# Performance work log

Hardware: AMD Instinct MI355X
Metric: run time of the kernel (lower is better)

The kernel has to match this reference:

```python
import jax, jax.numpy as jnp
import numpy as np

B, L, D_MODEL = 2, 4096, 1024
D_STATE, D_CONV, EXPAND, HEADDIM = 128, 4, 2, 64
D_INNER = EXPAND * D_MODEL              # 2048
NHEADS = D_INNER // HEADDIM             # 32
CONV_DIM = D_INNER + 2 * D_STATE        # 2304 (ngroups=1)
D_IN_PROJ = 2 * D_INNER + 2 * D_STATE + NHEADS  # 4384
CHUNK = 128
EPS = 1e-5


def _segsum(a):
    # a: (..., T) log-decays -> (..., T, T) lower-triangular segment sums, -inf above diagonal
    T = a.shape[-1]
    cs = jnp.cumsum(a, axis=-1)
    seg = cs[..., :, None] - cs[..., None, :]
    mask = jnp.tril(jnp.ones((T, T), dtype=bool))
    return jnp.where(mask, seg, -jnp.inf)


def _forward(x, norm_w, norm_b, in_proj_w, conv_w, conv_b, dt_bias, A_log, D, rms_w, out_proj_w):
    b, l, _ = x.shape
    # pre-LayerNorm
    mu = jnp.mean(x, -1, keepdims=True)
    var = jnp.mean(jnp.square(x - mu), -1, keepdims=True)
    xn = (x - mu) * jax.lax.rsqrt(var + EPS) * norm_w + norm_b
    zxbcdt = xn @ in_proj_w.T                              # (b,l,D_IN_PROJ)
    z = zxbcdt[..., :D_INNER]
    xBC = zxbcdt[..., D_INNER:D_INNER + CONV_DIM]
    dt = jax.nn.softplus(zxbcdt[..., -NHEADS:] + dt_bias)  # (b,l,h)
    # causal depthwise conv1d + SiLU over (x, B, C)
    xc = jnp.pad(xBC.transpose(0, 2, 1), ((0, 0), (0, 0), (D_CONV - 1, 0)))
    xc = jax.lax.conv_general_dilated(xc, conv_w[:, None, :], (1,), 'VALID',
                                      feature_group_count=CONV_DIM,
                                      dimension_numbers=('NCH', 'OIH', 'NCH'))
    xBC = jax.nn.silu(xc + conv_b[None, :, None]).transpose(0, 2, 1)
    xs = xBC[..., :D_INNER].reshape(b, l, NHEADS, HEADDIM)
    Bm = xBC[..., D_INNER:D_INNER + D_STATE]               # (b,l,n)
    Cm = xBC[..., D_INNER + D_STATE:]                      # (b,l,n)
    # SSD chunked selective scan
    A = -jnp.exp(A_log)                                    # (h,)
    a = dt * A                                             # (b,l,h) log decay
    X = xs * dt[..., None]                                 # (b,l,h,p)
    c = l // CHUNK
    a_c = a.reshape(b, c, CHUNK, NHEADS).transpose(0, 3, 1, 2)   # (b,h,c,s)
    a_cum = jnp.cumsum(a_c, -1)
    Lmat = jnp.exp(_segsum(a_c))                           # (b,h,c,s,s)
    Xc = X.reshape(b, c, CHUNK, NHEADS, HEADDIM)
    Bc = Bm.reshape(b, c, CHUNK, D_STATE)
    Cc = Cm.reshape(b, c, CHUNK, D_STATE)
    # intra-chunk (diagonal block) output
    Y_diag = jnp.einsum('bcln,bcsn,bhcls,bcshp->bclhp', Cc, Bc, Lmat, Xc)
    # chunk-final states
    decay_states = jnp.exp(a_cum[..., -1:] - a_cum)        # (b,h,c,s)
    states = jnp.einsum('bcln,bhcl,bclhp->bchpn', Bc, decay_states, Xc)
    states = jnp.concatenate([jnp.zeros_like(states[:, :1]), states], axis=1)
    chunk_decay = jnp.exp(_segsum(jnp.pad(a_cum[..., -1], ((0, 0), (0, 0), (1, 0)))))  # (b,h,c+1,c+1)
    prev = jnp.einsum('bhzc,bchpn->bzhpn', chunk_decay, states)[:, :-1]  # (b,c,h,p,n)
    # inter-chunk (off-diagonal) output
    Y_off = jnp.einsum('bcln,bchpn,bhcl->bclhp', Cc, prev, jnp.exp(a_cum))
    y = (Y_diag + Y_off).reshape(b, l, NHEADS, HEADDIM) + D[None, None, :, None] * xs
    y = y.reshape(b, l, D_INNER)
    # gated RMSNorm (norm_before_gate=False): norm(y * silu(z))
    y = y * jax.nn.silu(z)
    y = y * jax.lax.rsqrt(jnp.mean(jnp.square(y), -1, keepdims=True) + EPS) * rms_w
    return x + y @ out_proj_w.T


def setup_inputs() -> dict:
    key = jax.random.key(0)
    ks = jax.random.split(key, 8)
    return {
        'x': jax.random.normal(ks[0], (B, L, D_MODEL), jnp.float32),
        'norm_w': jnp.ones((D_MODEL,), jnp.float32),
        'norm_b': jnp.zeros((D_MODEL,), jnp.float32),
        'in_proj_w': 0.02 * jax.random.normal(ks[1], (D_IN_PROJ, D_MODEL), jnp.float32),
        'conv_w': 0.2 * jax.random.normal(ks[2], (CONV_DIM, D_CONV), jnp.float32),
        'conv_b': jnp.zeros((CONV_DIM,), jnp.float32),
        'dt_bias': jax.random.uniform(ks[3], (NHEADS,), jnp.float32, -4.0, 0.0),
        'A_log': jnp.log(jax.random.uniform(ks[4], (NHEADS,), jnp.float32, 1.0, 16.0)),
        'D': jnp.ones((NHEADS,), jnp.float32),
        'rms_w': jnp.ones((D_INNER,), jnp.float32),
        'out_proj_w': 0.02 * jax.random.normal(ks[5], (D_MODEL, D_INNER), jnp.float32),
    }


def reference(x, norm_w, norm_b, in_proj_w, conv_w, conv_b, dt_bias, A_log, D, rms_w, out_proj_w):
    return _forward(x, norm_w, norm_b, in_proj_w, conv_w, conv_b, dt_bias, A_log, D, rms_w, out_proj_w)
```

## Files before the change

### kernel.cpp

```cpp
#include <hip/hip_runtime.h>

#define B_ 2
#define L_ 4096
#define DMODEL 1024
#define DSTATE 128
#define DINNER 2048
#define NH 32
#define HD 64
#define DPROJ 4384
#define DPROJP 4480
#define NC 32
#define EPSF 1e-5f
#define ROWS (B_*L_)

typedef unsigned short u16;
typedef __attribute__((ext_vector_type(8))) short s8v;
typedef __attribute__((ext_vector_type(4))) float f4v;
typedef __attribute__((ext_vector_type(4))) int i4v;
typedef __attribute__((ext_vector_type(2))) int i2v;
typedef __attribute__((ext_vector_type(4))) float fl4;

static __device__ __forceinline__ float b2f(u16 u){
  unsigned int x = ((unsigned int)u) << 16;
  return __builtin_bit_cast(float, x);
}
static __device__ __forceinline__ u16 f2b(float f){
  unsigned int x = __builtin_bit_cast(unsigned int, f);
  unsigned int r = x + 0x7FFFu + ((x >> 16) & 1u);
  return (u16)(r >> 16);
}
static __device__ __forceinline__ float softplusf(float x){
  return (x > 20.f) ? x : log1pf(expf(x));
}
static __device__ __forceinline__ void gl_lds16(const u16* g, u16* l){
  __builtin_amdgcn_global_load_lds(
    (const __attribute__((address_space(1))) unsigned int*)g,
    (__attribute__((address_space(3))) unsigned int*)l, 16, 0, 0);
}
static __device__ __forceinline__ int swz(int row, int col){
  return row*128 + ((((col >> 3) ^ (row & 15)) << 3) | (col & 7));
}
static __device__ __forceinline__ int swz64(int row, int col){
  return row*64 + ((((col >> 3) ^ (row & 7)) << 3) | (col & 7));
}
static __device__ __forceinline__ int osw(int t, int j){
  return t*64 + ((((j >> 3) ^ ((t >> 3) & 7)) << 3) | (j & 7));
}

__global__ void k_dbg(float* out, float v){ out[0] = v; }

__global__ __launch_bounds__(256) void k_pack_w1(const float* __restrict__ W, u16* __restrict__ Wb){
  size_t i = (size_t)blockIdx.x*256 + threadIdx.x;
  if (i >= (size_t)DPROJP*DMODEL) return;
  size_t n = i / DMODEL;
  Wb[i] = (n < DPROJ) ? f2b(W[i]) : (u16)0;
}
__global__ __launch_bounds__(256) void k_pack_w2(const float* __restrict__ W, u16* __restrict__ Wb){
  size_t i = (size_t)blockIdx.x*256 + threadIdx.x;
  if (i >= (size_t)DMODEL*DINNER) return;
  Wb[i] = f2b(W[i]);
}

__global__ __launch_bounds__(256) void k_ln(const float* __restrict__ x, const float* __restrict__ nw,
                                            const float* __restrict__ nb, u16* __restrict__ xn){
  int m = blockIdx.x; int tid = threadIdx.x;
  const float* row = x + (size_t)m*DMODEL;
  fl4 v = *(const fl4*)&row[tid*4];
  float s1 = v[0]+v[1]+v[2]+v[3];
  float s2 = v[0]*v[0]+v[1]*v[1]+v[2]*v[2]+v[3]*v[3];
  #pragma unroll
  for (int o=32;o;o>>=1){ s1 += __shfl_down(s1,o); s2 += __shfl_down(s2,o); }
  __shared__ float r1[4], r2[4];
  if ((tid&63)==0){ r1[tid>>6]=s1; r2[tid>>6]=s2; }
  __syncthreads();
  s1 = r1[0]+r1[1]+r1[2]+r1[3]; s2 = r2[0]+r2[1]+r2[2]+r2[3];
  float mu = s1 * (1.f/DMODEL);
  float var = s2 * (1.f/DMODEL) - mu*mu;
  float rs = rsqrtf(var + EPSF);
  u16* o = xn + (size_t)m*DMODEL + tid*4;
  #pragma unroll
  for (int k=0;k<4;k++)
    o[k] = f2b((v[k]-mu)*rs*nw[tid*4+k] + nb[tid*4+k]);
}

template<int MODE>
__global__ __launch_bounds__(256) void k_gemm(const u16* __restrict__ A, const u16* __restrict__ Bw,
                  void* __restrict__ Cout, const float* __restrict__ resid,
                  int K, int lda, int ldb, int ldc){
  __shared__ u16 smem[2*128*64];
  u16* sA = smem;
  u16* sB = smem + 128*64;
  int tid = threadIdx.x;
  int ln = tid & 63, wid = tid >> 6;
  int wr = wid >> 1, wc = wid & 1;
  size_t m0 = (size_t)blockIdx.x * 128, n0 = (size_t)blockIdx.y * 128;
  int lrow = ln >> 3;
  f4v acc[4][4] = {};
  for (int k0 = 0; k0 < K; k0 += 64){
    #pragma unroll
    for (int i = 0; i < 4; ++i){
      int seg = wid*4 + i;
      int row = seg*8 + lrow;
      int scol = ((ln & 7) ^ (row & 7)) * 8;
      gl_lds16(&A [(m0+row)*lda + k0 + scol], &sA[seg*512]);
      gl_lds16(&Bw[(n0+row)*ldb + k0 + scol], &sB[seg*512]);
    }
    __syncthreads();
    #pragma unroll
    for (int kk=0; kk<2; kk++){
      s8v af[4], bfr[4];
      #pragma unroll
      for (int t=0;t<4;t++){
        int col = kk*32 + (ln>>4)*8;
        af[t]  = *(const s8v*)&sA[swz64(wr*64+t*16+(ln&15), col)];
        bfr[t] = *(const s8v*)&sB[swz64(wc*64+t*16+(ln&15), col)];
      }
      #pragma unroll
      for (int mt=0;mt<4;mt++)
        #pragma unroll
        for (int nt=0;nt<4;nt++)
          acc[mt][nt] = __builtin_amdgcn_mfma_f32_16x16x32_bf16(af[mt], bfr[nt], acc[mt][nt], 0,0,0);
    }
    __syncthreads();
  }
  if (MODE == 0){
    #pragma unroll
    for (int mt=0;mt<4;mt++)
      #pragma unroll
      for (int nt=0;nt<4;nt++)
        #pragma unroll
        for (int j=0;j<4;j++){
          int m = wr*64 + mt*16 + (ln>>4)*4 + j;
          int n = wc*64 + nt*16 + (ln&15);
          smem[m*128 + n] = f2b(acc[mt][nt][j]);
        }
    __syncthreads();
    #pragma unroll
    for (int it = 0; it < 8; ++it){
      int idx = (tid + it*256)*8;
      int row = idx >> 7, col = idx & 127;
      *(i4v*)&((u16*)Cout)[(m0+row)*ldc + n0 + col] = *(const i4v*)&smem[idx];
    }
  } else {
    #pragma unroll
    for (int mt=0;mt<4;mt++)
      #pragma unroll
      for (int nt=0;nt<4;nt++)
        #pragma unroll
        for (int j=0;j<4;j++){
          size_t m = m0 + wr*64 + mt*16 + (ln>>4)*4 + j;
          size_t n = n0 + wc*64 + nt*16 + (ln&15);
          ((float*)Cout)[m*ldc + n] = acc[mt][nt][j] + resid[m*ldc + n];
        }
  }
}

__global__ __launch_bounds__(256) void k_conv(const u16* __restrict__ zx, const float* __restrict__ cw,
    const float* __restrict__ cb, const float* __restrict__ dtb,
    u16* __restrict__ Xt, u16* __restrict__ Bln, u16* __restrict__ Bt,
    u16* __restrict__ Cln, float* __restrict__ dtg){
  __shared__ u16 in_s[131*64];
  __shared__ u16 out_s[128*64];
  __shared__ float dt_s[128];
  int bid = blockIdx.x;
  int g = bid % 36;
  int c = (bid / 36) & 31;
  int b = bid / (36*32);
  int tid = threadIdx.x;
  int t0 = c*128;
  size_t rowb = (size_t)b*L_ + t0;
  for (int i8 = tid; i8 < 1048; i8 += 256){
    int r = i8 >> 3, j0 = (i8 & 7)*8;
    int t = t0 - 3 + r;
    i4v v;
    if (t >= 0) v = *(const i4v*)&zx[((size_t)b*L_ + t)*DPROJP + 2048 + g*64 + j0];
    else { v[0]=0; v[1]=0; v[2]=0; v[3]=0; }
    *(i4v*)&in_s[r*64 + j0] = v;
  }
  if (g < 32 && tid < 128){
    float raw = b2f(zx[(rowb + tid)*DPROJP + (DPROJ - NH) + g]);
    float d = softplusf(raw + dtb[g]);
    dt_s[tid] = d;
    dtg[(size_t)(b*NH + g)*L_ + t0 + tid] = d;
  }
  __syncthreads();
  {
    int j = tid & 63;
    int ch = g*64 + j;
    float w0 = cw[ch*4+0], w1 = cw[ch*4+1], w2 = cw[ch*4+2], w3 = cw[ch*4+3];
    float bia = cb[ch];
    int tb = tid >> 6;
    #pragma unroll
    for (int it = 0; it < 32; ++it){
      int t = tb + it*4;
      float a = bia
        + w0*b2f(in_s[(t+0)*64 + j]) + w1*b2f(in_s[(t+1)*64 + j])
        + w2*b2f(in_s[(t+2)*64 + j]) + w3*b2f(in_s[(t+3)*64 + j]);
      out_s[osw(t, j)] = f2b(a / (1.f + __expf(-a)));
    }
  }
  __syncthreads();
  if (g < 32){
    for (int i = tid; i < 1024; i += 256){
      int j = i >> 4, tb = (i & 15)*8;
      i4v o; u16* ou = (u16*)&o;
      #pragma unroll
      for (int k = 0; k < 8; ++k)
        ou[k] = f2b(b2f(out_s[osw(tb + k, j)]) * dt_s[tb + k]);
      *(i4v*)&Xt[((size_t)((b*NH + g)*HD + j))*L_ + t0 + tb] = o;
    }
  } else {
    int q = g - 32;
    for (int i = tid; i < 1024; i += 256){
      int t = i >> 3, j0 = (i & 7)*8;
      i4v v = *(const i4v*)&out_s[osw(t, j0)];
      if (q < 2) *(i4v*)&Bln[(rowb + t)*DSTATE + q*64 + j0] = v;
      else       *(i4v*)&Cln[(rowb + t)*DSTATE + (q-2)*64 + j0] = v;
    }
    if (q < 2){
      for (int i = tid; i < 1024; i += 256){
        int j = i >> 4, tb = (i & 15)*8;
        i4v o; u16* ou = (u16*)&o;
        #pragma unroll
        for (int k = 0; k < 8; ++k) ou[k] = out_s[osw(tb + k, j)];
        *(i4v*)&Bt[((size_t)(b*DSTATE + q*64 + j))*L_ + t0 + tb] = o;
      }
    }
  }
}

__global__ __launch_bounds__(128) void k_acum(const float* __restrict__ dtg, const float* __restrict__ A_log,
                                              float* __restrict__ acum){
  int bid = blockIdx.x;
  int c = bid & 31, h = (bid >> 5) & 31, b = bid >> 10;
  int l = threadIdx.x;
  __shared__ float a[128];
  float Ah = -expf(A_log[h]);
  a[l] = dtg[(size_t)(b*NH + h)*L_ + c*128 + l] * Ah;
  __syncthreads();
  #pragma unroll
  for (int d = 1; d < 128; d <<= 1){
    float v = (l >= d) ? a[l-d] : 0.f;
    __syncthreads();
    a[l] += v;
    __syncthreads();
  }
  acum[(size_t)bid*128 + l] = a[l];
}

__global__ __launch_bounds__(256) void k_states(const u16* __restrict__ Xt, const u16* __restrict__ Bt,
    const float* __restrict__ acum, u16* __restrict__ states){
  __shared__ u16 sX[64*128];
  __shared__ u16 sB[128*128];
  __shared__ float dec[128];
  int bid = blockIdx.x;
  int h = bid & 31, c = (bid >> 5) & 31, b = bid >> 10;
  int tid = threadIdx.x;
  const float* acg = acum + ((size_t)((b*NH + h)*NC + c))*128;
  if (tid < 128) dec[tid] = __expf(acg[127] - acg[tid]);
  __syncthreads();
  const u16* xtb = Xt + ((size_t)((b*NH + h)*HD))*L_ + c*128;
  for (int i = tid*8; i < 64*128; i += 256*8){
    int p = i >> 7, l0 = i & 127;
    i4v v = *(const i4v*)&xtb[(size_t)p*L_ + l0];
    const u16* vu = (const u16*)&v;
    i4v o; u16* ou = (u16*)&o;
    #pragma unroll
    for (int j = 0; j < 8; ++j) ou[j] = f2b(b2f(vu[j]) * dec[l0 + j]);
    *(i4v*)&sX[swz(p, l0)] = o;
  }
  const u16* btb = Bt + (size_t)(b*DSTATE)*L_ + c*128;
  for (int i = tid*8; i < 128*128; i += 256*8){
    int n = i >> 7, l0 = i & 127;
    *(i4v*)&sB[swz(n, l0)] = *(const i4v*)&btb[(size_t)n*L_ + l0];
  }
  __syncthreads();
  int ln = tid & 63, wid = tid >> 6;
  int wr = wid >> 1, wc = wid & 1;
  f4v acc[2][4] = {};
  #pragma unroll
  for (int kk = 0; kk < 4; ++kk){
    s8v af[2], bfr[4];
    int col = kk*32 + (ln>>4)*8;
    #pragma unroll
    for (int t = 0; t < 2; ++t)
      af[t] = *(const s8v*)&sX[swz(wr*32 + t*16 + (ln&15), col)];
    #pragma unroll
    for (int t = 0; t < 4; ++t)
      bfr[t] = *(const s8v*)&sB[swz(wc*64 + t*16 + (ln&15), col)];
    #pragma unroll
    for (int mt = 0; mt < 2; ++mt)
      #pragma unroll
      for (int nt = 0; nt < 4; ++nt)
        acc[mt][nt] = __builtin_amdgcn_mfma_f32_16x16x32_bf16(af[mt], bfr[nt], acc[mt][nt], 0,0,0);
  }
  u16* out = states + ((size_t)((b*NC + c)*NH + h))*(HD*DSTATE);
  #pragma unroll
  for (int mt = 0; mt < 2; ++mt)
    #pragma unroll
    for (int nt = 0; nt < 4; ++nt){
      int n = wc*64 + nt*16 + (ln&15);
      #pragma unroll
      for (int j = 0; j < 4; ++j){
        int p = wr*32 + mt*16 + (ln>>4)*4 + j;
        out[(size_t)p*DSTATE + n] = f2b(acc[mt][nt][j]);
      }
    }
}

__global__ __launch_bounds__(256) void k_scan(u16* __restrict__ states, const float* __restrict__ acum){
  int bid = blockIdx.x;
  int eb = bid & 7;
  int hb = bid >> 3;
  int h = hb & 31, b = hb >> 5;
  int tid = threadIdx.x;
  size_t ebase = (size_t)eb*1024 + (size_t)tid*4;
  size_t hoff = ((size_t)(b*NC*NH + h))*(HD*DSTATE) + ebase;
  float dec[NC];
  #pragma unroll
  for (int c = 0; c < NC; ++c)
    dec[c] = __expf(acum[((size_t)((b*NH + h)*NC + c))*128 + 127]);
  i2v w[NC];
  #pragma unroll
  for (int c = 0; c < NC; ++c)
    w[c] = *(const i2v*)&states[(size_t)c*(NH*HD*DSTATE) + hoff];
  float run[4] = {0.f, 0.f, 0.f, 0.f};
  #pragma unroll
  for (int c = 0; c < NC; ++c){
    u16* wu = (u16*)&w[c];
    #pragma unroll
    for (int j = 0; j < 4; ++j){
      float tmp = b2f(wu[j]);
      wu[j] = f2b(run[j]);
      run[j] = run[j]*dec[c] + tmp;
    }
  }
  #pragma unroll
  for (int c = 0; c < NC; ++c)
    *(i2v*)&states[(size_t)c*(NH*HD*DSTATE) + hoff] = w[c];
}

__global__ __launch_bounds__(256) void k_y(const u16* __restrict__ Cln, const u16* __restrict__ Bln,
    const u16* __restrict__ Xt, const u16* __restrict__ prev, const float* __restrict__ acum,
    const float* __restrict__ dtg, const float* __restrict__ Dp, u16* __restrict__ Y){
  __shared__ u16 sC[128*128];
  __shared__ u16 sBS[128*128];
  __shared__ float dt_s[128];
  int bid = blockIdx.x;
  int h = bid & 31, c = (bid >> 5) & 31, b = bid >> 10;
  int tid = threadIdx.x;
  size_t rowb = (size_t)b*L_ + c*128;
  const float* acg = acum + ((size_t)((b*NH + h)*NC + c))*128;
  if (tid < 128) dt_s[tid] = dtg[(size_t)(b*NH + h)*L_ + c*128 + tid];
  for (int i = tid*8; i < 128*128; i += 256*8){
    int row = i >> 7, col = i & 127;
    int d = swz(row, col);
    *(i4v*)&sC[d]  = *(const i4v*)&Cln[(rowb + row)*DSTATE + col];
    *(i4v*)&sBS[d] = *(const i4v*)&Bln[(rowb + row)*DSTATE + col];
  }
  __syncthreads();
  int ln = tid & 63, wid = tid >> 6;
  int wr = wid >> 1, wc = wid & 1;
  float Dh = Dp[h];
  f4v aS[4][4] = {};
  #pragma unroll
  for (int kk = 0; kk < 4; ++kk){
    s8v af[4], bfr[4];
    #pragma unroll
    for (int t = 0; t < 4; ++t){
      int col = kk*32 + (ln>>4)*8;
      af[t]  = *(const s8v*)&sC [swz(wr*64 + t*16 + (ln&15), col)];
      bfr[t] = *(const s8v*)&sBS[swz(wc*64 + t*16 + (ln&15), col)];
    }
    #pragma unroll
    for (int mt = 0; mt < 4; ++mt)
      #pragma unroll
      for (int nt = 0; nt < 4; ++nt)
        aS[mt][nt] = __builtin_amdgcn_mfma_f32_16x16x32_bf16(af[mt], bfr[nt], aS[mt][nt], 0,0,0);
  }
  __syncthreads();
  #pragma unroll
  for (int mt = 0; mt < 4; ++mt)
    #pragma unroll
    for (int nt = 0; nt < 4; ++nt){
      int s = wc*64 + nt*16 + (ln&15);
      float as = acg[s];
      #pragma unroll
      for (int j = 0; j < 4; ++j){
        int l = wr*64 + mt*16 + (ln>>4)*4 + j;
        float v = 0.f;
        if (s <= l){
          v = aS[mt][nt][j] * __expf(acg[l] - as);
          if (s == l) v += Dh / dt_s[l];
        }
        sBS[swz(l, s)] = f2b(v);
      }
    }
  __syncthreads();
  const u16* xtb = Xt + ((size_t)((b*NH + h)*HD))*L_ + c*128;
  const u16* pv = prev + ((size_t)((b*NC + c)*NH + h))*(HD*DSTATE);
  f4v aD[4][2] = {}, aO[4][2] = {};
  #pragma unroll
  for (int kk = 0; kk < 4; ++kk){
    s8v aSf[4], aCf[4], bXf[2], bPf[2];
    #pragma unroll
    for (int t = 0; t < 4; ++t){
      int col = kk*32 + (ln>>4)*8;
      int row = wr*64 + t*16 + (ln&15);
      aSf[t] = *(const s8v*)&sBS[swz(row, col)];
      aCf[t] = *(const s8v*)&sC[swz(row, col)];
    }
    #pragma unroll
    for (int t = 0; t < 2; ++t){
      int p = wc*32 + t*16 + (ln&15);
      int ko = kk*32 + (ln>>4)*8;
      bXf[t] = *(const s8v*)&xtb[(size_t)p*L_ + ko];
      bPf[t] = *(const s8v*)&pv[(size_t)p*DSTATE + ko];
    }
    #pragma unroll
    for (int mt = 0; mt < 4; ++mt)
      #pragma unroll
      for (int nt = 0; nt < 2; ++nt){
        aD[mt][nt] = __builtin_amdgcn_mfma_f32_16x16x32_bf16(aSf[mt], bXf[nt], aD[mt][nt], 0,0,0);
        aO[mt][nt] = __builtin_amdgcn_mfma_f32_16x16x32_bf16(aCf[mt], bPf[nt], aO[mt][nt], 0,0,0);
      }
  }
  __syncthreads();
  #pragma unroll
  for (int mt = 0; mt < 4; ++mt)
    #pragma unroll
    for (int nt = 0; nt < 2; ++nt){
      int p = wc*32 + nt*16 + (ln&15);
      #pragma unroll
      for (int j = 0; j < 4; ++j){
        int l = wr*64 + mt*16 + (ln>>4)*4 + j;
        float ex = __expf(acg[l]);
        float yv = aD[mt][nt][j] + ex*aO[mt][nt][j];
        sC[l*64 + (p ^ ((l & 7) << 3))] = f2b(yv);
      }
    }
  __syncthreads();
  #pragma unroll
  for (int it = 0; it < 4; ++it){
    int idx = (tid + it*256)*8;
    int row = idx >> 6, col0 = idx & 63;
    i4v v = *(const i4v*)&sC[row*64 + (col0 ^ ((row & 7) << 3))];
    *(i4v*)&Y[(rowb + row)*DINNER + h*HD + col0] = v;
  }
}

__global__ __launch_bounds__(256) void k_gate(u16* __restrict__ Y, const u16* __restrict__ zx,
                                              const float* __restrict__ rw){
  size_t m = blockIdx.x; int tid = threadIdx.x;
  u16* yrow = Y + m*DINNER + tid*8;
  const u16* zrow = zx + m*DPROJP + tid*8;
  i4v yv = *(const i4v*)yrow;
  i4v zv = *(const i4v*)zrow;
  const u16* yu = (const u16*)&yv;
  const u16* zu = (const u16*)&zv;
  float yg[8]; float ss = 0.f;
  #pragma unroll
  for (int k = 0; k < 8; ++k){
    float z = b2f(zu[k]);
    float g = z / (1.f + __expf(-z));
    float v = b2f(yu[k]) * g;
    yg[k] = v; ss += v*v;
  }
  #pragma unroll
  for (int o = 32; o; o >>= 1) ss += __shfl_down(ss, o);
  __shared__ float r[4];
  if ((tid&63) == 0) r[tid>>6] = ss;
  __syncthreads();
  ss = r[0]+r[1]+r[2]+r[3];
  float rstd = rsqrtf(ss*(1.f/DINNER) + EPSF);
  #pragma unroll
  for (int k = 0; k < 8; ++k)
    yrow[k] = f2b(yg[k]*rstd*rw[tid*8+k]);
}

extern "C" void kernel_launch(void* const* d_in, const int* in_sizes, int n_in,
                              void* d_out, int out_size, void* d_ws, size_t ws_size,
                              hipStream_t stream){
  const float* x        = (const float*)d_in[0];
  const float* norm_w   = (const float*)d_in[1];
  const float* norm_b   = (const float*)d_in[2];
  const float* in_proj  = (const float*)d_in[3];
  const float* conv_w   = (const float*)d_in[4];
  const float* conv_b   = (const float*)d_in[5];
  const float* dt_bias  = (const float*)d_in[6];
  const float* A_log    = (const float*)d_in[7];
  const float* Dp       = (const float*)d_in[8];
  const float* rms_w    = (const float*)d_in[9];
  const float* out_proj = (const float*)d_in[10];

  char* ws = (char*)d_ws;
  size_t off = 0;
  auto alloc = [&](size_t bytes) -> void* {
    void* p = ws + off;
    off += (bytes + 255) & ~(size_t)255;
    return p;
  };
  u16*   w1b    = (u16*)  alloc((size_t)DPROJP*DMODEL*2);
  u16*   w2b    = (u16*)  alloc((size_t)DMODEL*DINNER*2);
  u16*   xn     = (u16*)  alloc((size_t)ROWS*DMODEL*2);
  u16*   zx     = (u16*)  alloc((size_t)ROWS*DPROJP*2);
  u16*   Xt     = (u16*)  alloc((size_t)B_*NH*HD*L_*2);
  u16*   Bln    = (u16*)  alloc((size_t)ROWS*DSTATE*2);
  u16*   Bt     = (u16*)  alloc((size_t)B_*DSTATE*L_*2);
  u16*   Cln    = (u16*)  alloc((size_t)ROWS*DSTATE*2);
  float* dtg    = (float*)alloc((size_t)B_*NH*L_*4);
  float* acum   = (float*)alloc((size_t)B_*NH*NC*128*4);
  u16*   Y      = (u16*)  alloc((size_t)ROWS*DINNER*2);
  u16* states = (u16*)d_out;
  if (off > ws_size){
    k_dbg<<<1, 1, 0, stream>>>((float*)d_out, (float)ws_size);
    return;
  }

  k_pack_w1<<<dim3((DPROJP*DMODEL + 255)/256), 256, 0, stream>>>(in_proj, w1b);
  k_pack_w2<<<dim3((DMODEL*DINNER + 255)/256), 256, 0, stream>>>(out_proj, w2b);
  k_ln<<<dim3(ROWS), 256, 0, stream>>>(x, norm_w, norm_b, xn);
  k_gemm<0><<<dim3(ROWS/128, DPROJP/128), 256, 0, stream>>>(xn, w1b, zx, nullptr,
                                                            DMODEL, DMODEL, DMODEL, DPROJP);
  k_conv<<<dim3(B_*NC*36), 256, 0, stream>>>(zx, conv_w, conv_b, dt_bias,
                                             Xt, Bln, Bt, Cln, dtg);
  k_acum<<<dim3(B_*NH*NC), 128, 0, stream>>>(dtg, A_log, acum);
  k_states<<<dim3(B_*NC*NH), 256, 0, stream>>>(Xt, Bt, acum, states);
  k_scan<<<dim3(B_*NH*8), 256, 0, stream>>>(states, acum);
  k_y<<<dim3(B_*NC*NH), 256, 0, stream>>>(Cln, Bln, Xt, states, acum, dtg, Dp, Y);
  k_gate<<<dim3(ROWS), 256, 0, stream>>>(Y, zx, rms_w);
  k_gemm<1><<<dim3(ROWS/128, DMODEL/128), 256, 0, stream>>>(Y, w2b, d_out, x,
                                                            DINNER, DINNER, DINNER, DMODEL);
}
```

Before: 307.1 us.

## Fuse weight packing and chunk cumsum; remap GEMM tiles across XCDs

The two weight-packing kernels become one launch, and the per-chunk cumulative decay scan moves from its own kernel into the conv kernel, which already computes dt. Both GEMMs switch to a 1D grid whose block index is remapped so that consecutive tiles land on the same XCD (8-way interleave), aiming for better L2 reuse of A and B panels. The conv kernel now carries extra barriers for the scan, and its four extra B/C blocks per chunk run the scan on zeros.

```diff
diff --git a/kernel.cpp b/kernel.cpp
--- a/kernel.cpp
+++ b/kernel.cpp
@@ -49,16 +49,18 @@
 
 __global__ void k_dbg(float* out, float v){ out[0] = v; }
 
-__global__ __launch_bounds__(256) void k_pack_w1(const float* __restrict__ W, u16* __restrict__ Wb){
+#define NW1 ((size_t)DPROJP*DMODEL)
+#define NW2 ((size_t)DMODEL*DINNER)
+__global__ __launch_bounds__(256) void k_pack(const float* __restrict__ W1, const float* __restrict__ W2,
+                                              u16* __restrict__ W1b, u16* __restrict__ W2b){
   size_t i = (size_t)blockIdx.x*256 + threadIdx.x;
-  if (i >= (size_t)DPROJP*DMODEL) return;
-  size_t n = i / DMODEL;
-  Wb[i] = (n < DPROJ) ? f2b(W[i]) : (u16)0;
-}
-__global__ __launch_bounds__(256) void k_pack_w2(const float* __restrict__ W, u16* __restrict__ Wb){
-  size_t i = (size_t)blockIdx.x*256 + threadIdx.x;
-  if (i >= (size_t)DMODEL*DINNER) return;
-  Wb[i] = f2b(W[i]);
+  if (i < NW1){
+    size_t n = i / DMODEL;
+    W1b[i] = (n < DPROJ) ? f2b(W1[i]) : (u16)0;
+  } else if (i < NW1 + NW2){
+    size_t j = i - NW1;
+    W2b[j] = f2b(W2[j]);
+  }
 }
 
 __global__ __launch_bounds__(256) void k_ln(const float* __restrict__ x, const float* __restrict__ nw,
@@ -83,17 +85,17 @@
     o[k] = f2b((v[k]-mu)*rs*nw[tid*4+k] + nb[tid*4+k]);
 }
 
-template<int MODE>
-__global__ __launch_bounds__(256) void k_gemm(const u16* __restrict__ A, const u16* __restrict__ Bw,
-                  void* __restrict__ Cout, const float* __restrict__ resid,
-                  int K, int lda, int ldb, int ldc){
+__global__ __launch_bounds__(256) void k_gemm_in(const u16* __restrict__ A, const u16* __restrict__ Bw,
+                  u16* __restrict__ Cout, int K, int lda, int ldb, int ldc, int nwg, int mtiles){
   __shared__ u16 smem[2*128*64];
   u16* sA = smem;
   u16* sB = smem + 128*64;
+  int cpx = nwg >> 3;
+  int lin = (blockIdx.x & 7)*cpx + (blockIdx.x >> 3);
   int tid = threadIdx.x;
   int ln = tid & 63, wid = tid >> 6;
   int wr = wid >> 1, wc = wid & 1;
-  size_t m0 = (size_t)blockIdx.x * 128, n0 = (size_t)blockIdx.y * 128;
+  size_t m0 = (size_t)(lin % mtiles) * 128, n0 = (size_t)(lin / mtiles) * 128;
   int lrow = ln >> 3;
   f4v acc[4][4] = {};
   for (int k0 = 0; k0 < K; k0 += 64){
@@ -123,45 +125,85 @@
     }
     __syncthreads();
   }
-  if (MODE == 0){
-    #pragma unroll
-    for (int mt=0;mt<4;mt++)
-      #pragma unroll
-      for (int nt=0;nt<4;nt++)
+  #pragma unroll
+  for (int mt=0;mt<4;mt++)
+    #pragma unroll
+    for (int nt=0;nt<4;nt++)
+      #pragma unroll
+      for (int j=0;j<4;j++){
+        int m = wr*64 + mt*16 + (ln>>4)*4 + j;
+        int n = wc*64 + nt*16 + (ln&15);
+        smem[m*128 + n] = f2b(acc[mt][nt][j]);
+      }
+  __syncthreads();
+  #pragma unroll
+  for (int it = 0; it < 8; ++it){
+    int idx = (tid + it*256)*8;
+    int row = idx >> 7, col = idx & 127;
+    *(i4v*)&Cout[(m0+row)*ldc + n0 + col] = *(const i4v*)&smem[idx];
+  }
+}
+
+__global__ __launch_bounds__(256) void k_gemm_out(const u16* __restrict__ A, const u16* __restrict__ Bw,
+                  float* __restrict__ Cout, const float* __restrict__ resid,
+                  int K, int lda, int ldb, int ldc, int nwg, int mtiles){
+  __shared__ u16 sA[128*64];
+  __shared__ u16 sB[128*64];
+  int cpx = nwg >> 3;
+  int lin = (blockIdx.x & 7)*cpx + (blockIdx.x >> 3);
+  int tid = threadIdx.x;
+  int ln = tid & 63, wid = tid >> 6;
+  int wr = wid >> 1, wc = wid & 1;
+  size_t m0 = (size_t)(lin % mtiles) * 128, n0 = (size_t)(lin / mtiles) * 128;
+  int lrow = ln >> 3;
+  f4v acc[4][4] = {};
+  for (int k0 = 0; k0 < K; k0 += 64){
+    #pragma unroll
+    for (int i = 0; i < 4; ++i){
+      int seg = wid*4 + i;
+      int row = seg*8 + lrow;
+      int scol = ((ln & 7) ^ (row & 7)) * 8;
+      gl_lds16(&A [(m0+row)*lda + k0 + scol], &sA[seg*512]);
+      gl_lds16(&Bw[(n0+row)*ldb + k0 + scol], &sB[seg*512]);
+    }
+    __syncthreads();
+    #pragma unroll
+    for (int kk=0; kk<2; kk++){
+      s8v af[4], bfr[4];
+      #pragma unroll
+      for (int t=0;t<4;t++){
+        int col = kk*32 + (ln>>4)*8;
+        af[t]  = *(const s8v*)&sA[swz64(wr*64+t*16+(ln&15), col)];
+        bfr[t] = *(const s8v*)&sB[swz64(wc*64+t*16+(ln&15), col)];
+      }
+      #pragma unroll
+      for (int mt=0;mt<4;mt++)
         #pragma unroll
-        for (int j=0;j<4;j++){
-          int m = wr*64 + mt*16 + (ln>>4)*4 + j;
-          int n = wc*64 + nt*16 + (ln&15);
-          smem[m*128 + n] = f2b(acc[mt][nt][j]);
-        }
+        for (int nt=0;nt<4;nt++)
+          acc[mt][nt] = __builtin_amdgcn_mfma_f32_16x16x32_bf16(af[mt], bfr[nt], acc[mt][nt], 0,0,0);
+    }
     __syncthreads();
-    #pragma unroll
-    for (int it = 0; it < 8; ++it){
-      int idx = (tid + it*256)*8;
-      int row = idx >> 7, col = idx & 127;
-      *(i4v*)&((u16*)Cout)[(m0+row)*ldc + n0 + col] = *(const i4v*)&smem[idx];
-    }
-  } else {
-    #pragma unroll
-    for (int mt=0;mt<4;mt++)
-      #pragma unroll
-      for (int nt=0;nt<4;nt++)
-        #pragma unroll
-        for (int j=0;j<4;j++){
-          size_t m = m0 + wr*64 + mt*16 + (ln>>4)*4 + j;
-          size_t n = n0 + wc*64 + nt*16 + (ln&15);
-          ((float*)Cout)[m*ldc + n] = acc[mt][nt][j] + resid[m*ldc + n];
-        }
-  }
+  }
+  #pragma unroll
+  for (int mt=0;mt<4;mt++)
+    #pragma unroll
+    for (int nt=0;nt<4;nt++)
+      #pragma unroll
+      for (int j=0;j<4;j++){
+        size_t m = m0 + wr*64 + mt*16 + (ln>>4)*4 + j;
+        size_t n = n0 + wc*64 + nt*16 + (ln&15);
+        Cout[m*ldc + n] = acc[mt][nt][j] + resid[m*ldc + n];
+      }
 }
 
 __global__ __launch_bounds__(256) void k_conv(const u16* __restrict__ zx, const float* __restrict__ cw,
-    const float* __restrict__ cb, const float* __restrict__ dtb,
+    const float* __restrict__ cb, const float* __restrict__ dtb, const float* __restrict__ A_log,
     u16* __restrict__ Xt, u16* __restrict__ Bln, u16* __restrict__ Bt,
-    u16* __restrict__ Cln, float* __restrict__ dtg){
+    u16* __restrict__ Cln, float* __restrict__ dtg, float* __restrict__ acum){
   __shared__ u16 in_s[131*64];
   __shared__ u16 out_s[128*64];
   __shared__ float dt_s[128];
+  __shared__ float a_s[128];
   int bid = blockIdx.x;
   int g = bid % 36;
   int c = (bid / 36) & 31;
@@ -177,13 +219,29 @@
     else { v[0]=0; v[1]=0; v[2]=0; v[3]=0; }
     *(i4v*)&in_s[r*64 + j0] = v;
   }
-  if (g < 32 && tid < 128){
-    float raw = b2f(zx[(rowb + tid)*DPROJP + (DPROJ - NH) + g]);
-    float d = softplusf(raw + dtb[g]);
-    dt_s[tid] = d;
-    dtg[(size_t)(b*NH + g)*L_ + t0 + tid] = d;
-  }
-  __syncthreads();
+  if (tid < 128){
+    if (g < 32){
+      float raw = b2f(zx[(rowb + tid)*DPROJP + (DPROJ - NH) + g]);
+      float d = softplusf(raw + dtb[g]);
+      dt_s[tid] = d;
+      dtg[(size_t)(b*NH + g)*L_ + t0 + tid] = d;
+      a_s[tid] = d * (-expf(A_log[g]));
+    } else {
+      dt_s[tid] = 0.f;
+      a_s[tid] = 0.f;
+    }
+  }
+  __syncthreads();
+  #pragma unroll
+  for (int d = 1; d < 128; d <<= 1){
+    float v = 0.f;
+    if (tid < 128 && tid >= d) v = a_s[tid - d];
+    __syncthreads();
+    if (tid < 128) a_s[tid] += v;
+    __syncthreads();
+  }
+  if (g < 32 && tid < 128)
+    acum[((size_t)((b*NH + g)*NC + c))*128 + tid] = a_s[tid];
   {
     int j = tid & 63;
     int ch = g*64 + j;
@@ -227,25 +285,6 @@
       }
     }
   }
-}
-
-__global__ __launch_bounds__(128) void k_acum(const float* __restrict__ dtg, const float* __restrict__ A_log,
-                                              float* __restrict__ acum){
-  int bid = blockIdx.x;
-  int c = bid & 31, h = (bid >> 5) & 31, b = bid >> 10;
-  int l = threadIdx.x;
-  __shared__ float a[128];
-  float Ah = -expf(A_log[h]);
-  a[l] = dtg[(size_t)(b*NH + h)*L_ + c*128 + l] * Ah;
-  __syncthreads();
-  #pragma unroll
-  for (int d = 1; d < 128; d <<= 1){
-    float v = (l >= d) ? a[l-d] : 0.f;
-    __syncthreads();
-    a[l] += v;
-    __syncthreads();
-  }
-  acum[(size_t)bid*128 + l] = a[l];
 }
 
 __global__ __launch_bounds__(256) void k_states(const u16* __restrict__ Xt, const u16* __restrict__ Bt,
@@ -517,18 +556,22 @@
     return;
   }
 
-  k_pack_w1<<<dim3((DPROJP*DMODEL + 255)/256), 256, 0, stream>>>(in_proj, w1b);
-  k_pack_w2<<<dim3((DMODEL*DINNER + 255)/256), 256, 0, stream>>>(out_proj, w2b);
+  k_pack<<<dim3((unsigned)((NW1 + NW2 + 255)/256)), 256, 0, stream>>>(in_proj, out_proj, w1b, w2b);
   k_ln<<<dim3(ROWS), 256, 0, stream>>>(x, norm_w, norm_b, xn);
-  k_gemm<0><<<dim3(ROWS/128, DPROJP/128), 256, 0, stream>>>(xn, w1b, zx, nullptr,
-                                                            DMODEL, DMODEL, DMODEL, DPROJP);
-  k_conv<<<dim3(B_*NC*36), 256, 0, stream>>>(zx, conv_w, conv_b, dt_bias,
-                                             Xt, Bln, Bt, Cln, dtg);
-  k_acum<<<dim3(B_*NH*NC), 128, 0, stream>>>(dtg, A_log, acum);
+  {
+    int nwg = (ROWS/128)*(DPROJP/128);
+    k_gemm_in<<<dim3(nwg), 256, 0, stream>>>(xn, w1b, zx, DMODEL, DMODEL, DMODEL, DPROJP,
+                                             nwg, ROWS/128);
+  }
+  k_conv<<<dim3(B_*NC*36), 256, 0, stream>>>(zx, conv_w, conv_b, dt_bias, A_log,
+                                             Xt, Bln, Bt, Cln, dtg, acum);
   k_states<<<dim3(B_*NC*NH), 256, 0, stream>>>(Xt, Bt, acum, states);
   k_scan<<<dim3(B_*NH*8), 256, 0, stream>>>(states, acum);
   k_y<<<dim3(B_*NC*NH), 256, 0, stream>>>(Cln, Bln, Xt, states, acum, dtg, Dp, Y);
   k_gate<<<dim3(ROWS), 256, 0, stream>>>(Y, zx, rms_w);
-  k_gemm<1><<<dim3(ROWS/128, DMODEL/128), 256, 0, stream>>>(Y, w2b, d_out, x,
-                                                            DINNER, DINNER, DINNER, DMODEL);
-}
+  {
+    int nwg = (ROWS/128)*(DMODEL/128);
+    k_gemm_out<<<dim3(nwg), 256, 0, stream>>>(Y, w2b, (float*)d_out, x,
+                                              DINNER, DINNER, DINNER, DMODEL, nwg, ROWS/128);
+  }
+}
```

Measured after the change: 323.9 us. +5.5%, slower.
